# Optimization experiments

Hardware: AMD Instinct MI355X
Metric: run time of the kernel (lower is better)

## Reference

```python
import jax, jax.numpy as jnp
import numpy as np

NUM_BEAM, NUM_NULL, NUM_BIN, NUM_CH = 8, 4, 257, 8
NUM_BLOCK, NUM_FRAME = 8, 500
ALPHA, LOW_FREQ, HIGH_FREQ = 0.35, 5, 70


def setup_inputs() -> dict:
    key = jax.random.key(0)
    k1, k2, k3, k4 = jax.random.split(key, 4)
    return {
        "input": jax.random.normal(k1, (NUM_BLOCK, NUM_FRAME, 2, NUM_BIN, NUM_CH), jnp.float32),
        "beam_id": jax.random.randint(k2, (NUM_BLOCK,), 0, NUM_BEAM),
        "targ_w": jax.random.normal(k3, (NUM_BEAM, 2, NUM_BIN, NUM_CH), jnp.float32),
        "null_w": jax.random.normal(k4, (NUM_BEAM, NUM_NULL, 2, NUM_BIN, NUM_CH), jnp.float32),
    }


def _forward(input, beam_id, targ_w, null_w):
    a = ALPHA
    xr, xi = input[:, :, 0], input[:, :, 1]            # (B,T,F,C)
    # target beamformer: select per-block complex weights (B,2,F,C)
    tw = targ_w[beam_id]
    twr, twi = tw[:, 0], tw[:, 1]                      # (B,F,C)
    tr = jnp.einsum('btfc,bfc->btf', xr, twr) - jnp.einsum('btfc,bfc->btf', xi, twi)
    ti = jnp.einsum('btfc,bfc->btf', xr, twi) + jnp.einsum('btfc,bfc->btf', xi, twr)
    tr, ti = tr[..., None], ti[..., None]              # (B,T,F,1)
    # null beamformer: (B,N,2,F,C)
    nw = null_w[beam_id]
    nwr, nwi = nw[:, :, 0], nw[:, :, 1]                # (B,N,F,C)
    nr = jnp.einsum('btfc,bnfc->btfn', xr, nwr) - jnp.einsum('btfc,bnfc->btfn', xi, nwi)
    ni = jnp.einsum('btfc,bnfc->btfn', xr, nwi) + jnp.einsum('btfc,bnfc->btfn', xi, nwr)
    # elementwise cross-spectra products (B,T,F,N)
    pr = tr * nr + ti * ni
    pi = ti * nr - tr * ni
    pw = jnp.mean(xr ** 2 + xi ** 2, axis=-1, keepdims=True)  # (B,T,F,1)

    # t = 0 (note: (1-alpha) scales only the FIRST product, as in the source)
    phi_r0 = (1.0 - a) * tr[:, 0] * nr[:, 0] + ti[:, 0] * ni[:, 0]
    phi_i0 = (1.0 - a) * ti[:, 0] * nr[:, 0] - tr[:, 0] * ni[:, 0]
    psd0 = (1.0 - a) * pw[:, 0]
    phi0 = jnp.sqrt(phi_r0 ** 2 + phi_i0 ** 2)
    dcf0 = jnp.clip(phi0 / (psd0 + 1e-13), 0.01, 1.0)

    def step(carry, xs):
        phi_r, phi_i, psd = carry
        pr_t, pi_t, pw_t = xs
        phi_r = a * phi_r + (1.0 - a) * pr_t
        phi_i = a * phi_i + (1.0 - a) * pi_t
        psd = a * psd + (1.0 - a) * pw_t
        phi = jnp.sqrt(phi_r ** 2 + phi_i ** 2)
        dcf_t = jnp.clip(phi / (psd + 1e-13), 0.01, 1.0)
        pre = jnp.sum(psd[:, LOW_FREQ:HIGH_FREQ, :], axis=1, keepdims=True)
        aft = jnp.sum(phi[:, LOW_FREQ:HIGH_FREQ, :], axis=1, keepdims=True)
        ratio = jnp.clip(aft / (pre + 1e-10), 0.01, 1.0)
        dcf_t = jnp.sqrt(dcf_t * ratio)
        return (phi_r, phi_i, psd), dcf_t

    xs = (jnp.moveaxis(pr[:, 1:], 1, 0),
          jnp.moveaxis(pi[:, 1:], 1, 0),
          jnp.moveaxis(pw[:, 1:], 1, 0))
    _, dcf_rest = jax.lax.scan(step, (phi_r0, phi_i0, psd0), xs)  # (T-1,B,F,N)
    dcf = jnp.concatenate([dcf0[None], dcf_rest], axis=0)
    dcf = jnp.moveaxis(dcf, 0, 1)                                 # (B,T,F,N)
    targ_out = jnp.stack([tr[..., 0], ti[..., 0]], axis=2)        # (B,T,2,F)
    return dcf, targ_out


def reference(input, beam_id, targ_w, null_w):
    return _forward(input, beam_id, targ_w, null_w)
```

## Files before the change

kernel.cpp:

```cpp
#include <hip/hip_runtime.h>

#define NB 8
#define NT 500
#define NF 257
#define NC 8
#define NNUL 4
#define LOWF 5
#define HIGHF 70
#define S_CHUNK 8
#define WARM 4
#define N_CHUNK 63
#define AL 0.35f

__device__ __forceinline__ float dot8(const float4& a0, const float4& a1,
                                      const float4& b0, const float4& b1) {
    return a0.x*b0.x + a0.y*b0.y + a0.z*b0.z + a0.w*b0.w
         + a1.x*b1.x + a1.y*b1.y + a1.z*b1.z + a1.w*b1.w;
}

__global__ __launch_bounds__(512, 2) void dcf_ema_kernel(
    const float* __restrict__ x,
    const int* __restrict__ beam_id,
    const float* __restrict__ targ_w,
    const float* __restrict__ null_w,
    float* __restrict__ out,
    float* __restrict__ ws)
{
    const int tid = threadIdx.x;
    const int bid = blockIdx.x;
    const int fh = bid & 1;
    const int b  = (bid >> 1) & 7;
    const int k  = bid >> 4;
    const int t0 = k * S_CHUNK;
    const int te = min(NT, t0 + S_CHUNK);
    int ts = t0 - WARM; if (ts < 0) ts = 0;

    const int f = fh * 128 + (tid >> 2);
    const int n = tid & 3;
    const int wid = tid >> 6;
    const int lane = tid & 63;
    const bool extra = (fh == 1) && (tid < 4);

    __shared__ float s_w256[16 + 4 * 16];

    const int beam = beam_id[b];
    const int pA = n & 1;
    const int offA = pA * (NF * NC);
    const int offB = (1 - pA) * (NF * NC);
    const int psel = (n == 1 || n == 2) ? 1 : 0;
    const float nsign = pA ? -1.f : 1.f;

    float4 tw0, tw1, nwA0, nwA1, nwB0, nwB1;
    {
        const float* tp = targ_w + ((size_t)(beam * 2 + psel) * NF + f) * NC;
        tw0 = *(const float4*)(tp);  tw1 = *(const float4*)(tp + 4);
        const float* qp = null_w + ((size_t)((beam * NNUL + n) * 2) * NF + f) * NC;
        nwA0 = *(const float4*)(qp + offA);  nwA1 = *(const float4*)(qp + offA + 4);
        nwB0 = *(const float4*)(qp + offB);  nwB1 = *(const float4*)(qp + offB + 4);
    }
    if (tid < 16) {
        int p = tid >> 3, c = tid & 7;
        s_w256[tid] = targ_w[((size_t)(beam * 2 + p) * NF + 256) * NC + c];
    } else if (tid < 80) {
        int i = tid - 16;
        int nn = i >> 4, p = (i >> 3) & 1, c = i & 7;
        s_w256[tid] = null_w[((size_t)((beam * NNUL + nn) * 2 + p) * NF + 256) * NC + c];
    }
    __syncthreads();

    float phi_r = 0.f, phi_i = 0.f, psd = 0.f;
    float phi_r2 = 0.f, phi_i2 = 0.f, psd2 = 0.f;
    const float a = AL, oma = 1.0f - AL;
    const size_t rowlen = 2 * NF * NC;
    const bool in_red = (f >= LOWF) && (f < HIGHF);

    const float* xrow = x + (size_t)(b * NT + ts) * rowlen + f * NC;
    float4 pA0 = *(const float4*)(xrow + offA);
    float4 pA1 = *(const float4*)(xrow + offA + 4);
    float4 pB0 = *(const float4*)(xrow + offB);
    float4 pB1 = *(const float4*)(xrow + offB + 4);

    float* outT = out + (size_t)NB * NT * NF * NNUL;

    for (int t = ts; t < te; ++t) {
        const float4 A0 = pA0, A1 = pA1, B0 = pB0, B1 = pB1;
        if (t + 1 < te) {
            const float* xr2 = x + (size_t)(b * NT + t + 1) * rowlen + f * NC;
            pA0 = *(const float4*)(xr2 + offA);
            pA1 = *(const float4*)(xr2 + offA + 4);
            pB0 = *(const float4*)(xr2 + offB);
            pB1 = *(const float4*)(xr2 + offB + 4);
        }

        const float d = dot8(A0, A1, tw0, tw1);
        const float e = __shfl_xor(d, 1);
        const float u = (n < 2) ? ((n == 0) ? (d - e) : (e - d)) : (d + e);
        const float v = __shfl_xor(u, 2);
        const float tr = (n < 2) ? u : v;
        const float ti = (n < 2) ? v : u;

        const float P = dot8(A0, A1, nwA0, nwA1);
        const float Q = dot8(B0, B1, nwB0, nwB1);
        const float nr = nsign * (P - Q);
        const float ni = dot8(A0, A1, nwB0, nwB1) + dot8(B0, B1, nwA0, nwA1);
        const float pw = (dot8(A0, A1, A0, A1) + dot8(B0, B1, B0, B1)) * 0.125f;

        if (t == 0) {
            phi_r = oma * tr * nr + ti * ni;
            phi_i = oma * ti * nr - tr * ni;
            psd   = oma * pw;
        } else {
            phi_r = a * phi_r + oma * (tr * nr + ti * ni);
            phi_i = a * phi_i + oma * (ti * nr - tr * ni);
            psd   = a * psd + oma * pw;
        }

        float tr2 = 0.f, ti2 = 0.f;
        if (extra) {
            const float* xw = x + (size_t)(b * NT + t) * rowlen + 256 * NC;
            const float4 eA0 = *(const float4*)(xw + offA);
            const float4 eA1 = *(const float4*)(xw + offA + 4);
            const float4 eB0 = *(const float4*)(xw + offB);
            const float4 eB1 = *(const float4*)(xw + offB + 4);
            const float4 etw0 = *(const float4*)&s_w256[psel * 8];
            const float4 etw1 = *(const float4*)&s_w256[psel * 8 + 4];
            const float* nq = &s_w256[16 + n * 16];
            const float4 enA0 = *(const float4*)(nq + pA * 8);
            const float4 enA1 = *(const float4*)(nq + pA * 8 + 4);
            const float4 enB0 = *(const float4*)(nq + (1 - pA) * 8);
            const float4 enB1 = *(const float4*)(nq + (1 - pA) * 8 + 4);
            const float d2 = dot8(eA0, eA1, etw0, etw1);
            const float e2 = __shfl_xor(d2, 1);
            const float u2 = (n < 2) ? ((n == 0) ? (d2 - e2) : (e2 - d2)) : (d2 + e2);
            const float v2 = __shfl_xor(u2, 2);
            tr2 = (n < 2) ? u2 : v2;
            ti2 = (n < 2) ? v2 : u2;
            const float P2 = dot8(eA0, eA1, enA0, enA1);
            const float Q2 = dot8(eB0, eB1, enB0, enB1);
            const float nr2 = nsign * (P2 - Q2);
            const float ni2 = dot8(eA0, eA1, enB0, enB1) + dot8(eB0, eB1, enA0, enA1);
            const float pw2 = (dot8(eA0, eA1, eA0, eA1) + dot8(eB0, eB1, eB0, eB1)) * 0.125f;
            if (t == 0) {
                phi_r2 = oma * tr2 * nr2 + ti2 * ni2;
                phi_i2 = oma * ti2 * nr2 - tr2 * ni2;
                psd2   = oma * pw2;
            } else {
                phi_r2 = a * phi_r2 + oma * (tr2 * nr2 + ti2 * ni2);
                phi_i2 = a * phi_i2 + oma * (ti2 * nr2 - tr2 * ni2);
                psd2   = a * psd2 + oma * pw2;
            }
        }

        if (t >= t0) {
            const float phi = sqrtf(phi_r * phi_r + phi_i * phi_i);
            const float dcfv = fminf(fmaxf(phi / (psd + 1e-13f), 0.01f), 1.0f);
            const size_t bt = (size_t)(b * NT + t);
            out[(bt * NF + f) * NNUL + n] = dcfv;
            if (n == 0) outT[(bt * 2 + 0) * NF + f] = tr;
            if (n == 1) outT[(bt * 2 + 1) * NF + f] = ti;
            if (extra) {
                const float phi2 = sqrtf(phi_r2 * phi_r2 + phi_i2 * phi_i2);
                const float dcf2v = fminf(fmaxf(phi2 / (psd2 + 1e-13f), 0.01f), 1.0f);
                out[(bt * NF + 256) * NNUL + n] = dcf2v;
                if (n == 0) outT[(bt * 2 + 0) * NF + 256] = tr2;
                if (n == 1) outT[(bt * 2 + 1) * NF + 256] = ti2;
            }
            if (fh == 0 && t >= 1 && wid < 5) {
                float v_phi = in_red ? phi : 0.f;
                float v_psd = (in_red && n == 0) ? psd : 0.f;
                #pragma unroll
                for (int off = 4; off < 64; off <<= 1) {
                    v_phi += __shfl_xor(v_phi, off);
                    v_psd += __shfl_xor(v_psd, off);
                }
                float* cell = ws + bt * 5;
                if (lane < 4) atomicAdd(cell + lane, v_phi);
                if (lane == 0) atomicAdd(cell + 4, v_psd);
            }
        }
    }
}

__global__ __launch_bounds__(256) void dcf_ratio_kernel(
    float* __restrict__ out, const float* __restrict__ ws)
{
    const int bt = blockIdx.x;
    if ((bt % NT) == 0) return;
    __shared__ float s_ratio[4];
    if (threadIdx.x < 4) {
        const float pre = ws[bt * 5 + 4];
        const float aft = ws[bt * 5 + threadIdx.x];
        s_ratio[threadIdx.x] = fminf(fmaxf(aft / (pre + 1e-10f), 0.01f), 1.0f);
    }
    __syncthreads();
    const float r0 = s_ratio[0], r1 = s_ratio[1], r2 = s_ratio[2], r3 = s_ratio[3];
    float4* dcf = (float4*)(out + (size_t)bt * (NF * NNUL));
    for (int i = threadIdx.x; i < NF; i += 256) {
        float4 v = dcf[i];
        v.x = sqrtf(v.x * r0);
        v.y = sqrtf(v.y * r1);
        v.z = sqrtf(v.z * r2);
        v.w = sqrtf(v.w * r3);
        dcf[i] = v;
    }
}

extern "C" void kernel_launch(void* const* d_in, const int* in_sizes, int n_in,
                              void* d_out, int out_size, void* d_ws, size_t ws_size,
                              hipStream_t stream) {
    const float* x       = (const float*)d_in[0];
    const int*   beam_id = (const int*)d_in[1];
    const float* targ_w  = (const float*)d_in[2];
    const float* null_w  = (const float*)d_in[3];
    float* out           = (float*)d_out;
    float* ws            = (float*)d_ws;

    hipMemsetAsync(ws, 0, (size_t)NB * NT * 5 * sizeof(float), stream);
    dcf_ema_kernel<<<dim3(NB * N_CHUNK * 2), dim3(512), 0, stream>>>(
        x, beam_id, targ_w, null_w, out, ws);
    dcf_ratio_kernel<<<dim3(NB * NT), dim3(256), 0, stream>>>(out, ws);
}
```

Measured before the change: 141.8 us.

## Fuse ratio pass into EMA kernel with in-block shared-memory reduction

Each block now covers all 256 frequency rows with 1024 threads. The low/high-frequency reductions run in shared memory with double-buffered partials and a barrier per time step, and the ratio/sqrt scaling is applied before the single dcf store. This removes the workspace memset, the global atomics and the second kernel that reread and rewrote the dcf output. The cost is a __syncthreads per timestep across 16 waves and half as many blocks, each larger.

```diff
diff --git a/kernel.cpp b/kernel.cpp
--- a/kernel.cpp
+++ b/kernel.cpp
@@ -18,30 +18,29 @@
          + a1.x*b1.x + a1.y*b1.y + a1.z*b1.z + a1.w*b1.w;
 }
 
-__global__ __launch_bounds__(512, 2) void dcf_ema_kernel(
+__global__ __launch_bounds__(1024, 4) void dcf_fused_kernel(
     const float* __restrict__ x,
     const int* __restrict__ beam_id,
     const float* __restrict__ targ_w,
     const float* __restrict__ null_w,
-    float* __restrict__ out,
-    float* __restrict__ ws)
+    float* __restrict__ out)
 {
     const int tid = threadIdx.x;
     const int bid = blockIdx.x;
-    const int fh = bid & 1;
-    const int b  = (bid >> 1) & 7;
-    const int k  = bid >> 4;
+    const int b  = bid & 7;
+    const int k  = bid >> 3;
     const int t0 = k * S_CHUNK;
     const int te = min(NT, t0 + S_CHUNK);
     int ts = t0 - WARM; if (ts < 0) ts = 0;
 
-    const int f = fh * 128 + (tid >> 2);
+    const int f = tid >> 2;
     const int n = tid & 3;
     const int wid = tid >> 6;
     const int lane = tid & 63;
-    const bool extra = (fh == 1) && (tid < 4);
+    const bool extra = (tid < 4);
 
     __shared__ float s_w256[16 + 4 * 16];
+    __shared__ float s_part[2][25];
 
     const int beam = beam_id[b];
     const int pA = n & 1;
@@ -153,55 +152,43 @@
 
         if (t >= t0) {
             const float phi = sqrtf(phi_r * phi_r + phi_i * phi_i);
-            const float dcfv = fminf(fmaxf(phi / (psd + 1e-13f), 0.01f), 1.0f);
+            float dcfv = fminf(fmaxf(phi / (psd + 1e-13f), 0.01f), 1.0f);
             const size_t bt = (size_t)(b * NT + t);
-            out[(bt * NF + f) * NNUL + n] = dcfv;
             if (n == 0) outT[(bt * 2 + 0) * NF + f] = tr;
             if (n == 1) outT[(bt * 2 + 1) * NF + f] = ti;
+            float dcf2v = 0.f;
             if (extra) {
                 const float phi2 = sqrtf(phi_r2 * phi_r2 + phi_i2 * phi_i2);
-                const float dcf2v = fminf(fmaxf(phi2 / (psd2 + 1e-13f), 0.01f), 1.0f);
-                out[(bt * NF + 256) * NNUL + n] = dcf2v;
+                dcf2v = fminf(fmaxf(phi2 / (psd2 + 1e-13f), 0.01f), 1.0f);
                 if (n == 0) outT[(bt * 2 + 0) * NF + 256] = tr2;
                 if (n == 1) outT[(bt * 2 + 1) * NF + 256] = ti2;
             }
-            if (fh == 0 && t >= 1 && wid < 5) {
-                float v_phi = in_red ? phi : 0.f;
-                float v_psd = (in_red && n == 0) ? psd : 0.f;
-                #pragma unroll
-                for (int off = 4; off < 64; off <<= 1) {
-                    v_phi += __shfl_xor(v_phi, off);
-                    v_psd += __shfl_xor(v_psd, off);
+
+            if (t >= 1) {
+                if (wid < 5) {
+                    float v_phi = in_red ? phi : 0.f;
+                    float v_psd = (in_red && n == 0) ? psd : 0.f;
+                    #pragma unroll
+                    for (int off = 4; off < 64; off <<= 1) {
+                        v_phi += __shfl_xor(v_phi, off);
+                        v_psd += __shfl_xor(v_psd, off);
+                    }
+                    float* cell = s_part[t & 1];
+                    if (lane < 4)  cell[wid * 5 + lane] = v_phi;
+                    if (lane == 0) cell[wid * 5 + 4]    = v_psd;
                 }
-                float* cell = ws + bt * 5;
-                if (lane < 4) atomicAdd(cell + lane, v_phi);
-                if (lane == 0) atomicAdd(cell + 4, v_psd);
+                __syncthreads();
+                const float* sp = s_part[t & 1];
+                const float pre = sp[4] + sp[9] + sp[14] + sp[19] + sp[24];
+                const float aft = sp[n] + sp[5 + n] + sp[10 + n] + sp[15 + n] + sp[20 + n];
+                const float ratio = fminf(fmaxf(aft / (pre + 1e-10f), 0.01f), 1.0f);
+                dcfv = sqrtf(dcfv * ratio);
+                if (extra) dcf2v = sqrtf(dcf2v * ratio);
             }
-        }
-    }
-}
-
-__global__ __launch_bounds__(256) void dcf_ratio_kernel(
-    float* __restrict__ out, const float* __restrict__ ws)
-{
-    const int bt = blockIdx.x;
-    if ((bt % NT) == 0) return;
-    __shared__ float s_ratio[4];
-    if (threadIdx.x < 4) {
-        const float pre = ws[bt * 5 + 4];
-        const float aft = ws[bt * 5 + threadIdx.x];
-        s_ratio[threadIdx.x] = fminf(fmaxf(aft / (pre + 1e-10f), 0.01f), 1.0f);
-    }
-    __syncthreads();
-    const float r0 = s_ratio[0], r1 = s_ratio[1], r2 = s_ratio[2], r3 = s_ratio[3];
-    float4* dcf = (float4*)(out + (size_t)bt * (NF * NNUL));
-    for (int i = threadIdx.x; i < NF; i += 256) {
-        float4 v = dcf[i];
-        v.x = sqrtf(v.x * r0);
-        v.y = sqrtf(v.y * r1);
-        v.z = sqrtf(v.z * r2);
-        v.w = sqrtf(v.w * r3);
-        dcf[i] = v;
+
+            out[(bt * NF + f) * NNUL + n] = dcfv;
+            if (extra) out[(bt * NF + 256) * NNUL + n] = dcf2v;
+        }
     }
 }
 
@@ -213,10 +200,8 @@
     const float* targ_w  = (const float*)d_in[2];
     const float* null_w  = (const float*)d_in[3];
     float* out           = (float*)d_out;
-    float* ws            = (float*)d_ws;
-
-    hipMemsetAsync(ws, 0, (size_t)NB * NT * 5 * sizeof(float), stream);
-    dcf_ema_kernel<<<dim3(NB * N_CHUNK * 2), dim3(512), 0, stream>>>(
-        x, beam_id, targ_w, null_w, out, ws);
-    dcf_ratio_kernel<<<dim3(NB * NT), dim3(256), 0, stream>>>(out, ws);
+    (void)d_ws; (void)ws_size;
+
+    dcf_fused_kernel<<<dim3(NB * N_CHUNK), dim3(1024), 0, stream>>>(
+        x, beam_id, targ_w, null_w, out);
 }
```

After: 136.5 us. -3.7%, faster.
